# Kernel optimization log

Measured on AMD Instinct MI355X. Metric: run time of the kernel, lower is better.

## Reference

```python
import jax, jax.numpy as jnp
import numpy as np

K_DIM = 1024
HEADS = 16
D_K = K_DIM // HEADS


def setup_inputs() -> dict:
    key = jax.random.key(0)
    ks = jax.random.split(key, 6)
    b, t, k = 4, 1024, K_DIM
    scale = 1.0 / np.sqrt(k)
    return {
        "x": jax.random.normal(ks[0], (b, t, k), dtype=jnp.float32),
        "Wq": jax.random.normal(ks[1], (k, k), dtype=jnp.float32) * scale,
        "Wk": jax.random.normal(ks[2], (k, k), dtype=jnp.float32) * scale,
        "Wv": jax.random.normal(ks[3], (k, k), dtype=jnp.float32) * scale,
        "Wo": jax.random.normal(ks[4], (k, k), dtype=jnp.float32) * scale,
        "bo": jax.random.normal(ks[5], (k,), dtype=jnp.float32) * 0.01,
    }


def reference(x, Wq, Wk, Wv, Wo, bo):
    b, t, k = x.shape
    h, d_k = HEADS, D_K
    # Linear(k,k) applies x @ W.T; project then split heads -> [b, h, t, d_k]
    Q = (x @ Wq.T).reshape(b, t, h, d_k).transpose(0, 2, 1, 3)
    Kh = (x @ Wk.T).reshape(b, t, h, d_k).transpose(0, 2, 1, 3)
    V = (x @ Wv.T).reshape(b, t, h, d_k).transpose(0, 2, 1, 3)
    scores = jnp.einsum("bhqd,bhkd->bhqk", Q, Kh) / jnp.sqrt(jnp.float32(d_k))
    attn = jax.nn.softmax(scores, axis=-1)
    out = jnp.einsum("bhqk,bhkd->bhqd", attn, V)
    out = out.transpose(0, 2, 1, 3).reshape(b, t, k)
    return out @ Wo.T + bo
```

## Files before the change

### kernel.cpp

```cpp
#include <hip/hip_runtime.h>
#include <hip/hip_bf16.h>

typedef __attribute__((ext_vector_type(4))) float f32x4;
typedef __attribute__((ext_vector_type(8))) short short8;

#define B_   4
#define T_   1024
#define H_   16
#define DK_  64
#define KDIM 1024

__device__ __forceinline__ unsigned short f2bf(float f){
  union { float f; unsigned int u; } a; a.f = f;
  unsigned int u = a.u;
  return (unsigned short)((u + 0x7FFFu + ((u >> 16) & 1u)) >> 16);
}

__device__ __forceinline__ void gload16(const void* g, void* l){
  __builtin_amdgcn_global_load_lds(
      (const __attribute__((address_space(1))) unsigned int*)g,
      (__attribute__((address_space(3))) unsigned int*)l,
      16, 0, 0);
}

__global__ __launch_bounds__(256) void convert5(
    const float* __restrict__ x,  const float* __restrict__ wq,
    const float* __restrict__ wk, const float* __restrict__ wv,
    const float* __restrict__ wo,
    short* __restrict__ xb,  short* __restrict__ wqb,
    short* __restrict__ wkb, short* __restrict__ wvb, short* __restrict__ wob)
{
  int i = blockIdx.x * 256 + threadIdx.x;
  const float* s; short* d; int off;
  if (i < (1 << 20)) { s = x; d = xb; off = i; }
  else {
    int j = i - (1 << 20);
    int w = j >> 18;
    off = j & ((1 << 18) - 1);
    s = (w == 0) ? wq : (w == 1) ? wk : (w == 2) ? wv : wo;
    d = (w == 0) ? wqb : (w == 1) ? wkb : (w == 2) ? wvb : wob;
  }
  float4 v = ((const float4*)s)[off];
  ushort4 o;
  o.x = f2bf(v.x); o.y = f2bf(v.y); o.z = f2bf(v.z); o.w = f2bf(v.w);
  ((ushort4*)d)[off] = o;
}

__device__ __forceinline__ void gemm_core(const short* __restrict__ A,
                                          const short* __restrict__ W,
                                          int m0, int n0,
                                          short* Als, short* Bls,
                                          f32x4 acc[4][4])
{
  const int tid = threadIdx.x;
  const int wv = tid >> 6, lane = tid & 63;
  const int lr = lane & 15, lq = lane >> 4;
  const int wr = wv >> 1, wc = wv & 1;
#pragma unroll
  for (int m = 0; m < 4; ++m)
#pragma unroll
    for (int n = 0; n < 4; ++n) acc[m][n] = (f32x4){0.f, 0.f, 0.f, 0.f};

  const int r0 = tid >> 2;
  const int c0 = (tid & 3) * 8;

  auto stage = [&](int buf, int ks) {
    const int k0 = ks * 32;
#pragma unroll
    for (int p = 0; p < 2; ++p) {
      const int r = p * 64 + r0;
      const short* ga = A + (size_t)(m0 + r) * KDIM + k0 + c0;
      const short* gb = W + (size_t)(n0 + r) * KDIM + k0 + c0;
      short* la = Als + buf * 4096 + p * 2048 + wv * 512;
      short* lb = Bls + buf * 4096 + p * 2048 + wv * 512;
      gload16(ga, la);
      gload16(gb, lb);
    }
  };

  stage(0, 0);
  __syncthreads();
  for (int ks = 0; ks < 32; ++ks) {
    const int cur = ks & 1;
    if (ks + 1 < 32) stage(cur ^ 1, ks + 1);
    const short* Ab = Als + cur * 4096;
    const short* Bb = Bls + cur * 4096;
    short8 af[4], bfr[4];
#pragma unroll
    for (int i = 0; i < 4; ++i) {
      af[i]  = *(const short8*)(Ab + (wr * 64 + i * 16 + lr) * 32 + lq * 8);
      bfr[i] = *(const short8*)(Bb + (wc * 64 + i * 16 + lr) * 32 + lq * 8);
    }
#pragma unroll
    for (int m = 0; m < 4; ++m)
#pragma unroll
      for (int n = 0; n < 4; ++n)
        acc[m][n] = __builtin_amdgcn_mfma_f32_16x16x32_bf16(af[m], bfr[n], acc[m][n], 0, 0, 0);
    __syncthreads();
  }
}

__global__ __launch_bounds__(256, 2) void gemm_qkv(
    const short* __restrict__ xb,
    const short* __restrict__ Wqb, const short* __restrict__ Wkb, const short* __restrict__ Wvb,
    short* __restrict__ Qb, short* __restrict__ Kb, short* __restrict__ VTb)
{
  __shared__ short Als[2 * 4096];
  __shared__ short Bls[2 * 4096];
  const int m0 = blockIdx.x * 128;
  const int by = blockIdx.y;
  const int wsel = by >> 3;
  const int n0 = (by & 7) * 128;
  const short* W = (wsel == 0) ? Wqb : (wsel == 1) ? Wkb : Wvb;
  f32x4 acc[4][4];
  gemm_core(xb, W, m0, n0, Als, Bls, acc);

  const int tid = threadIdx.x, lane = tid & 63, wv = tid >> 6;
  const int lr = lane & 15, lq = lane >> 4, wr = wv >> 1, wc = wv & 1;
  if (wsel < 2) {
    short* O = wsel ? Kb : Qb;
#pragma unroll
    for (int m = 0; m < 4; ++m)
#pragma unroll
      for (int n = 0; n < 4; ++n)
#pragma unroll
        for (int j = 0; j < 4; ++j) {
          int row = m0 + wr * 64 + m * 16 + lq * 4 + j;
          int col = n0 + wc * 64 + n * 16 + lr;
          O[(size_t)row * KDIM + col] = (short)f2bf(acc[m][n][j]);
        }
  } else {
#pragma unroll
    for (int m = 0; m < 4; ++m)
#pragma unroll
      for (int n = 0; n < 4; ++n) {
        int row = m0 + wr * 64 + m * 16 + lq * 4;
        int col = n0 + wc * 64 + n * 16 + lr;
        int b = row >> 10, t = row & 1023, h = col >> 6, d = col & 63;
        ushort4 v;
        v.x = f2bf(acc[m][n][0]); v.y = f2bf(acc[m][n][1]);
        v.z = f2bf(acc[m][n][2]); v.w = f2bf(acc[m][n][3]);
        *(ushort4*)&VTb[(size_t)((b * 16 + h) * 64 + d) * 1024 + t] = v;
      }
  }
}

__global__ __launch_bounds__(256) void attn_kern(
    const short* __restrict__ Qb, const short* __restrict__ Kb,
    const short* __restrict__ VTb, short* __restrict__ AOb)
{
  __shared__ short kl[64 * 64];
  __shared__ short vl[64 * 64];
  __shared__ short pl[4][16 * 64];
  const int bh = blockIdx.y;
  const int b = bh >> 4, h = bh & 15;
  const int q0 = blockIdx.x * 64;
  const int tid = threadIdx.x;
  const int wv = tid >> 6, lane = tid & 63;
  const int lr = lane & 15, lq = lane >> 4;

  const short* Qrow = Qb + (size_t)(b * T_ + q0 + wv * 16 + lr) * KDIM + h * DK_;
  short8 qf[2];
  qf[0] = *(const short8*)(Qrow + lq * 8);
  qf[1] = *(const short8*)(Qrow + 32 + lq * 8);

  float m_r[4] = {-1e30f, -1e30f, -1e30f, -1e30f};
  float l_r[4] = {0.f, 0.f, 0.f, 0.f};
  f32x4 oacc[4];
#pragma unroll
  for (int i = 0; i < 4; ++i) oacc[i] = (f32x4){0.f, 0.f, 0.f, 0.f};

  const int skr = tid >> 3;
  const int skc = (tid & 7) * 8;

  for (int kt = 0; kt < 16; ++kt) {
    const int kv0 = kt * 64;
#pragma unroll
    for (int p = 0; p < 2; ++p) {
      const int kr = p * 32 + skr;
      const int sc = skc ^ ((kr & 7) << 3);
      uint4 kval = *(const uint4*)(Kb + (size_t)(b * T_ + kv0 + kr) * KDIM + h * DK_ + skc);
      *(uint4*)&kl[kr * 64 + sc] = kval;
      uint4 vval = *(const uint4*)(VTb + (size_t)((b * 16 + h) * 64 + kr) * 1024 + kv0 + skc);
      *(uint4*)&vl[kr * 64 + sc] = vval;
    }
    __syncthreads();

    f32x4 s[4];
#pragma unroll
    for (int nt = 0; nt < 4; ++nt) {
      s[nt] = (f32x4){0.f, 0.f, 0.f, 0.f};
#pragma unroll
      for (int kk = 0; kk < 2; ++kk) {
        const int krow = nt * 16 + lr;
        const int cb = (kk * 32 + lq * 8) ^ ((krow & 7) << 3);
        short8 bfrag = *(const short8*)(kl + krow * 64 + cb);
        s[nt] = __builtin_amdgcn_mfma_f32_16x16x32_bf16(qf[kk], bfrag, s[nt], 0, 0, 0);
      }
    }

#pragma unroll
    for (int j = 0; j < 4; ++j) {
      float s0 = s[0][j] * 0.125f, s1 = s[1][j] * 0.125f;
      float s2 = s[2][j] * 0.125f, s3 = s[3][j] * 0.125f;
      float mx = fmaxf(fmaxf(s0, s1), fmaxf(s2, s3));
      mx = fmaxf(mx, __shfl_xor(mx, 1));
      mx = fmaxf(mx, __shfl_xor(mx, 2));
      mx = fmaxf(mx, __shfl_xor(mx, 4));
      mx = fmaxf(mx, __shfl_xor(mx, 8));
      const float mn = fmaxf(m_r[j], mx);
      const float al = __expf(m_r[j] - mn);
      m_r[j] = mn;
      float p0 = __expf(s0 - mn), p1 = __expf(s1 - mn);
      float p2 = __expf(s2 - mn), p3 = __expf(s3 - mn);
      float rs = p0 + p1 + p2 + p3;
      rs += __shfl_xor(rs, 1);
      rs += __shfl_xor(rs, 2);
      rs += __shfl_xor(rs, 4);
      rs += __shfl_xor(rs, 8);
      l_r[j] = l_r[j] * al + rs;
#pragma unroll
      for (int nt = 0; nt < 4; ++nt) oacc[nt][j] *= al;
      const int pr = lq * 4 + j;
      const int swz = (pr & 7) << 3;
      pl[wv][pr * 64 + ((0 * 16 + lr) ^ swz)] = (short)f2bf(p0);
      pl[wv][pr * 64 + ((1 * 16 + lr) ^ swz)] = (short)f2bf(p1);
      pl[wv][pr * 64 + ((2 * 16 + lr) ^ swz)] = (short)f2bf(p2);
      pl[wv][pr * 64 + ((3 * 16 + lr) ^ swz)] = (short)f2bf(p3);
    }
    __syncthreads();

    short8 pf[2];
#pragma unroll
    for (int kk = 0; kk < 2; ++kk)
      pf[kk] = *(const short8*)(pl[wv] + lr * 64 + ((kk * 32 + lq * 8) ^ ((lr & 7) << 3)));
#pragma unroll
    for (int nt = 0; nt < 4; ++nt) {
#pragma unroll
      for (int kk = 0; kk < 2; ++kk) {
        const int vrow = nt * 16 + lr;
        const int cb = (kk * 32 + lq * 8) ^ ((vrow & 7) << 3);
        short8 vf = *(const short8*)(vl + vrow * 64 + cb);
        oacc[nt] = __builtin_amdgcn_mfma_f32_16x16x32_bf16(pf[kk], vf, oacc[nt], 0, 0, 0);
      }
    }
    __syncthreads();
  }

#pragma unroll
  for (int nt = 0; nt < 4; ++nt) {
#pragma unroll
    for (int j = 0; j < 4; ++j) {
      const int row = q0 + wv * 16 + lq * 4 + j;
      const int col = h * DK_ + nt * 16 + lr;
      AOb[(size_t)(b * T_ + row) * KDIM + col] = (short)f2bf(oacc[nt][j] / l_r[j]);
    }
  }
}

__global__ __launch_bounds__(256, 2) void gemm_out(
    const short* __restrict__ AOb, const short* __restrict__ Wob,
    const float* __restrict__ bias, float* __restrict__ out)
{
  __shared__ short Als[2 * 4096];
  __shared__ short Bls[2 * 4096];
  const int m0 = blockIdx.x * 128;
  const int n0 = blockIdx.y * 128;
  f32x4 acc[4][4];
  gemm_core(AOb, Wob, m0, n0, Als, Bls, acc);

  const int tid = threadIdx.x, lane = tid & 63, wv = tid >> 6;
  const int lr = lane & 15, lq = lane >> 4, wr = wv >> 1, wc = wv & 1;
#pragma unroll
  for (int m = 0; m < 4; ++m)
#pragma unroll
    for (int n = 0; n < 4; ++n) {
      int col = n0 + wc * 64 + n * 16 + lr;
      float bv = bias[col];
#pragma unroll
      for (int j = 0; j < 4; ++j) {
        int row = m0 + wr * 64 + m * 16 + lq * 4 + j;
        out[(size_t)row * KDIM + col] = acc[m][n][j] + bv;
      }
    }
}

extern "C" void kernel_launch(void* const* d_in, const int* in_sizes, int n_in,
                              void* d_out, int out_size, void* d_ws, size_t ws_size,
                              hipStream_t stream) {
  const float* x  = (const float*)d_in[0];
  const float* Wq = (const float*)d_in[1];
  const float* Wk = (const float*)d_in[2];
  const float* Wv = (const float*)d_in[3];
  const float* Wo = (const float*)d_in[4];
  const float* bo = (const float*)d_in[5];

  short* ws = (short*)d_ws;
  short* xb  = ws;
  short* Wqb = ws + 4194304;
  short* Wkb = ws + 5242880;
  short* Wvb = ws + 6291456;
  short* Wob = ws + 7340032;
  short* Qb  = ws + 8388608;
  short* Kb  = ws + 12582912;
  short* VTb = ws + 16777216;
  short* AOb = ws + 20971520;

  convert5<<<8192, 256, 0, stream>>>(x, Wq, Wk, Wv, Wo, xb, Wqb, Wkb, Wvb, Wob);
  gemm_qkv<<<dim3(32, 24), 256, 0, stream>>>(xb, Wqb, Wkb, Wvb, Qb, Kb, VTb);
  attn_kern<<<dim3(16, 64), 256, 0, stream>>>(Qb, Kb, VTb, AOb);
  gemm_out<<<dim3(32, 8), 256, 0, stream>>>(AOb, Wob, bo, (float*)d_out);
}
```

Baseline: 198.5 us.

## Double-buffer attention K/V tiles via async LDS loads with transposed MFMA and lazy rescale

The attention kernel now loads 128-key K/V tiles into double-buffered LDS with global_load_lds, so the next tile's load overlaps compute on the current one. It swaps the MFMA operand order so each lane owns a single query row, which turns the per-row max and sum reductions into two cross-lane shuffles. Q is pre-scaled by log2(e)/sqrt(d_k) in the projection epilogue so the softmax can use exp2. The running max is only updated when it grows by more than 8, which skips most rescales of the accumulator. The costs are more LDS use, per-wave barrier removal that relies on an s_waitcnt, a stray empty loop, and looser exponent bounds from the lazy rescale.

Result: faster. 186.1 us (-6.2%).

```diff
diff --git a/kernel.cpp b/kernel.cpp
--- a/kernel.cpp
+++ b/kernel.cpp
@@ -10,10 +10,18 @@
 #define DK_  64
 #define KDIM 1024
 
+#define QSCALE 0.18033688011112042f
+
 __device__ __forceinline__ unsigned short f2bf(float f){
   union { float f; unsigned int u; } a; a.f = f;
   unsigned int u = a.u;
   return (unsigned short)((u + 0x7FFFu + ((u >> 16) & 1u)) >> 16);
+}
+
+__device__ __forceinline__ unsigned short f2bf_rn(float f){
+  union { __hip_bfloat16 h; unsigned short u; } cv;
+  cv.h = __float2bfloat16(f);
+  return cv.u;
 }
 
 __device__ __forceinline__ void gload16(const void* g, void* l){
@@ -119,6 +127,7 @@
   const int lr = lane & 15, lq = lane >> 4, wr = wv >> 1, wc = wv & 1;
   if (wsel < 2) {
     short* O = wsel ? Kb : Qb;
+    const float sc = wsel ? 1.0f : QSCALE;
 #pragma unroll
     for (int m = 0; m < 4; ++m)
 #pragma unroll
@@ -127,7 +136,7 @@
         for (int j = 0; j < 4; ++j) {
           int row = m0 + wr * 64 + m * 16 + lq * 4 + j;
           int col = n0 + wc * 64 + n * 16 + lr;
-          O[(size_t)row * KDIM + col] = (short)f2bf(acc[m][n][j]);
+          O[(size_t)row * KDIM + col] = (short)f2bf(acc[m][n][j] * sc);
         }
   } else {
 #pragma unroll
@@ -149,112 +158,142 @@
     const short* __restrict__ Qb, const short* __restrict__ Kb,
     const short* __restrict__ VTb, short* __restrict__ AOb)
 {
-  __shared__ short kl[64 * 64];
-  __shared__ short vl[64 * 64];
-  __shared__ short pl[4][16 * 64];
-  const int bh = blockIdx.y;
-  const int b = bh >> 4, h = bh & 15;
+  __shared__ __align__(16) short kl[2][128 * 64];
+  __shared__ __align__(16) short vl[2][64 * 128];
+  __shared__ __align__(16) short pl[4][16 * 64];
+  const int bh = blockIdx.y, b = bh >> 4, h = bh & 15;
   const int q0 = blockIdx.x * 64;
-  const int tid = threadIdx.x;
-  const int wv = tid >> 6, lane = tid & 63;
+  const int tid = threadIdx.x, wv = tid >> 6, lane = tid & 63;
   const int lr = lane & 15, lq = lane >> 4;
 
   const short* Qrow = Qb + (size_t)(b * T_ + q0 + wv * 16 + lr) * KDIM + h * DK_;
-  short8 qf[2];
-  qf[0] = *(const short8*)(Qrow + lq * 8);
-  qf[1] = *(const short8*)(Qrow + 32 + lq * 8);
-
-  float m_r[4] = {-1e30f, -1e30f, -1e30f, -1e30f};
-  float l_r[4] = {0.f, 0.f, 0.f, 0.f};
+  short8 qf0 = *(const short8*)(Qrow + lq * 8);
+  short8 qf1 = *(const short8*)(Qrow + 32 + lq * 8);
+
+  const short* Kbase = Kb + (size_t)(b * T_) * KDIM + h * DK_;
+  const short* Vbase = VTb + (size_t)(bh * DK_) * 1024;
+
+  const int krow_ = tid >> 3, kcol_ = (tid & 7) * 8;
+  const int vrow_ = tid >> 4, vcol_ = (tid & 15) * 8;
+
+  auto stage = [&](int buf, int kv0) {
+#pragma unroll
+    for (int p = 0; p < 4; ++p) {
+      const int r = p * 32 + krow_;
+      gload16(Kbase + (size_t)(kv0 + r) * KDIM + (kcol_ ^ ((r & 7) << 3)),
+              &kl[buf][p * 2048 + wv * 512]);
+    }
+#pragma unroll
+    for (int p = 0; p < 4; ++p) {
+      const int r = p * 16 + vrow_;
+      gload16(Vbase + (size_t)r * 1024 + kv0 + (vcol_ ^ ((r & 7) << 3)),
+              &vl[buf][p * 2048 + wv * 512]);
+    }
+  };
+
   f32x4 oacc[4];
 #pragma unroll
   for (int i = 0; i < 4; ++i) oacc[i] = (f32x4){0.f, 0.f, 0.f, 0.f};
-
-  const int skr = tid >> 3;
-  const int skc = (tid & 7) * 8;
-
-  for (int kt = 0; kt < 16; ++kt) {
-    const int kv0 = kt * 64;
-#pragma unroll
-    for (int p = 0; p < 2; ++p) {
-      const int kr = p * 32 + skr;
-      const int sc = skc ^ ((kr & 7) << 3);
-      uint4 kval = *(const uint4*)(Kb + (size_t)(b * T_ + kv0 + kr) * KDIM + h * DK_ + skc);
-      *(uint4*)&kl[kr * 64 + sc] = kval;
-      uint4 vval = *(const uint4*)(VTb + (size_t)((b * 16 + h) * 64 + kr) * 1024 + kv0 + skc);
-      *(uint4*)&vl[kr * 64 + sc] = vval;
+  float m_r = -1e30f, l_r = 0.f;
+  const int swq = (lr & 7) << 3;
+  short* plw = pl[wv];
+
+  int cur = 0;
+  stage(0, 0);
+  __syncthreads();
+
+  for (int kt = 0; kt < 16384 / (128 * 1024 / T_); ++kt) { }
+
+  for (int kt = 0; kt < 8; ++kt) {
+    if (kt < 7) stage(cur ^ 1, (kt + 1) * 128);
+
+    f32x4 s[8];
+#pragma unroll
+    for (int nt = 0; nt < 8; ++nt) {
+      const int kr = nt * 16 + lr;
+      const int sw = (kr & 7) << 3;
+      short8 kf0 = *(const short8*)&kl[cur][kr * 64 + ((lq * 8) ^ sw)];
+      short8 kf1 = *(const short8*)&kl[cur][kr * 64 + ((32 + lq * 8) ^ sw)];
+      f32x4 z = (f32x4){0.f, 0.f, 0.f, 0.f};
+      z = __builtin_amdgcn_mfma_f32_16x16x32_bf16(kf0, qf0, z, 0, 0, 0);
+      s[nt] = __builtin_amdgcn_mfma_f32_16x16x32_bf16(kf1, qf1, z, 0, 0, 0);
+    }
+
+    float t0, t1, mx;
+    {
+      float a0 = fmaxf(fmaxf(s[0][0], s[0][1]), fmaxf(s[0][2], s[0][3]));
+      float a1 = fmaxf(fmaxf(s[1][0], s[1][1]), fmaxf(s[1][2], s[1][3]));
+      float a2 = fmaxf(fmaxf(s[2][0], s[2][1]), fmaxf(s[2][2], s[2][3]));
+      float a3 = fmaxf(fmaxf(s[3][0], s[3][1]), fmaxf(s[3][2], s[3][3]));
+      float a4 = fmaxf(fmaxf(s[4][0], s[4][1]), fmaxf(s[4][2], s[4][3]));
+      float a5 = fmaxf(fmaxf(s[5][0], s[5][1]), fmaxf(s[5][2], s[5][3]));
+      float a6 = fmaxf(fmaxf(s[6][0], s[6][1]), fmaxf(s[6][2], s[6][3]));
+      float a7 = fmaxf(fmaxf(s[7][0], s[7][1]), fmaxf(s[7][2], s[7][3]));
+      t0 = fmaxf(fmaxf(a0, a1), fmaxf(a2, a3));
+      t1 = fmaxf(fmaxf(a4, a5), fmaxf(a6, a7));
+      mx = fmaxf(t0, t1);
+    }
+    mx = fmaxf(mx, __shfl_xor(mx, 16));
+    mx = fmaxf(mx, __shfl_xor(mx, 32));
+    if (!__all(mx <= m_r + 8.f)) {
+      const float mn = fmaxf(m_r, mx);
+      const float al = exp2f(m_r - mn);
+      l_r *= al;
+#pragma unroll
+      for (int nt = 0; nt < 4; ++nt)
+#pragma unroll
+        for (int j = 0; j < 4; ++j) oacc[nt][j] *= al;
+      m_r = mn;
+    }
+    float rs = 0.f;
+#pragma unroll
+    for (int nt = 0; nt < 8; ++nt)
+#pragma unroll
+      for (int j = 0; j < 4; ++j) {
+        float e = exp2f(s[nt][j] - m_r);
+        s[nt][j] = e;
+        rs += e;
+      }
+    rs += __shfl_xor(rs, 16);
+    rs += __shfl_xor(rs, 32);
+    l_r += rs;
+
+#pragma unroll
+    for (int half = 0; half < 2; ++half) {
+#pragma unroll
+      for (int nt = 0; nt < 4; ++nt) {
+        f32x4 v = s[half * 4 + nt];
+        ushort4 u;
+        u.x = f2bf_rn(v[0]); u.y = f2bf_rn(v[1]);
+        u.z = f2bf_rn(v[2]); u.w = f2bf_rn(v[3]);
+        *(ushort4*)&plw[lr * 64 + ((nt * 16 + lq * 4) ^ swq)] = u;
+      }
+      asm volatile("s_waitcnt lgkmcnt(0)" ::: "memory");
+      short8 pf0 = *(const short8*)&plw[lr * 64 + ((lq * 8) ^ swq)];
+      short8 pf1 = *(const short8*)&plw[lr * 64 + ((32 + lq * 8) ^ swq)];
+#pragma unroll
+      for (int ntd = 0; ntd < 4; ++ntd) {
+        const int vr = ntd * 16 + lr;
+        const int sw = (vr & 7) << 3;
+        short8 vf0 = *(const short8*)&vl[cur][vr * 128 + ((half * 64 + lq * 8) ^ sw)];
+        short8 vf1 = *(const short8*)&vl[cur][vr * 128 + ((half * 64 + 32 + lq * 8) ^ sw)];
+        oacc[ntd] = __builtin_amdgcn_mfma_f32_16x16x32_bf16(vf0, pf0, oacc[ntd], 0, 0, 0);
+        oacc[ntd] = __builtin_amdgcn_mfma_f32_16x16x32_bf16(vf1, pf1, oacc[ntd], 0, 0, 0);
+      }
     }
     __syncthreads();
-
-    f32x4 s[4];
-#pragma unroll
-    for (int nt = 0; nt < 4; ++nt) {
-      s[nt] = (f32x4){0.f, 0.f, 0.f, 0.f};
-#pragma unroll
-      for (int kk = 0; kk < 2; ++kk) {
-        const int krow = nt * 16 + lr;
-        const int cb = (kk * 32 + lq * 8) ^ ((krow & 7) << 3);
-        short8 bfrag = *(const short8*)(kl + krow * 64 + cb);
-        s[nt] = __builtin_amdgcn_mfma_f32_16x16x32_bf16(qf[kk], bfrag, s[nt], 0, 0, 0);
-      }
-    }
-
-#pragma unroll
-    for (int j = 0; j < 4; ++j) {
-      float s0 = s[0][j] * 0.125f, s1 = s[1][j] * 0.125f;
-      float s2 = s[2][j] * 0.125f, s3 = s[3][j] * 0.125f;
-      float mx = fmaxf(fmaxf(s0, s1), fmaxf(s2, s3));
-      mx = fmaxf(mx, __shfl_xor(mx, 1));
-      mx = fmaxf(mx, __shfl_xor(mx, 2));
-      mx = fmaxf(mx, __shfl_xor(mx, 4));
-      mx = fmaxf(mx, __shfl_xor(mx, 8));
-      const float mn = fmaxf(m_r[j], mx);
-      const float al = __expf(m_r[j] - mn);
-      m_r[j] = mn;
-      float p0 = __expf(s0 - mn), p1 = __expf(s1 - mn);
-      float p2 = __expf(s2 - mn), p3 = __expf(s3 - mn);
-      float rs = p0 + p1 + p2 + p3;
-      rs += __shfl_xor(rs, 1);
-      rs += __shfl_xor(rs, 2);
-      rs += __shfl_xor(rs, 4);
-      rs += __shfl_xor(rs, 8);
-      l_r[j] = l_r[j] * al + rs;
-#pragma unroll
-      for (int nt = 0; nt < 4; ++nt) oacc[nt][j] *= al;
-      const int pr = lq * 4 + j;
-      const int swz = (pr & 7) << 3;
-      pl[wv][pr * 64 + ((0 * 16 + lr) ^ swz)] = (short)f2bf(p0);
-      pl[wv][pr * 64 + ((1 * 16 + lr) ^ swz)] = (short)f2bf(p1);
-      pl[wv][pr * 64 + ((2 * 16 + lr) ^ swz)] = (short)f2bf(p2);
-      pl[wv][pr * 64 + ((3 * 16 + lr) ^ swz)] = (short)f2bf(p3);
-    }
-    __syncthreads();
-
-    short8 pf[2];
-#pragma unroll
-    for (int kk = 0; kk < 2; ++kk)
-      pf[kk] = *(const short8*)(pl[wv] + lr * 64 + ((kk * 32 + lq * 8) ^ ((lr & 7) << 3)));
-#pragma unroll
-    for (int nt = 0; nt < 4; ++nt) {
-#pragma unroll
-      for (int kk = 0; kk < 2; ++kk) {
-        const int vrow = nt * 16 + lr;
-        const int cb = (kk * 32 + lq * 8) ^ ((vrow & 7) << 3);
-        short8 vf = *(const short8*)(vl + vrow * 64 + cb);
-        oacc[nt] = __builtin_amdgcn_mfma_f32_16x16x32_bf16(pf[kk], vf, oacc[nt], 0, 0, 0);
-      }
-    }
-    __syncthreads();
-  }
-
+    cur ^= 1;
+  }
+
+  const float inv = 1.0f / l_r;
 #pragma unroll
   for (int nt = 0; nt < 4; ++nt) {
-#pragma unroll
-    for (int j = 0; j < 4; ++j) {
-      const int row = q0 + wv * 16 + lq * 4 + j;
-      const int col = h * DK_ + nt * 16 + lr;
-      AOb[(size_t)(b * T_ + row) * KDIM + col] = (short)f2bf(oacc[nt][j] / l_r[j]);
-    }
+    ushort4 u;
+    u.x = f2bf_rn(oacc[nt][0] * inv);
+    u.y = f2bf_rn(oacc[nt][1] * inv);
+    u.z = f2bf_rn(oacc[nt][2] * inv);
+    u.w = f2bf_rn(oacc[nt][3] * inv);
+    *(ushort4*)&AOb[(size_t)(b * T_ + q0 + wv * 16 + lr) * KDIM + h * DK_ + nt * 16 + lq * 4] = u;
   }
 }
 
```
